# Optimization experiments

Measured on AMD Instinct MI355X. Metric: run time of the kernel, lower is better.

Reference implementation:

```python
import jax, jax.numpy as jnp
import numpy as np

B, S, D_MODEL, H = 4, 2048, 2048, 16
HD = D_MODEL // H  # 128
ROPE_BASE = 10000.0


def apply_rope(x):
    # x: [B, H, S, HD]; interleaved-pair rotary embedding along seq axis
    s, d = x.shape[2], x.shape[3]
    inv_freq = 1.0 / (ROPE_BASE ** (jnp.arange(0, d, 2, dtype=jnp.float32) / d))  # [d/2]
    ang = jnp.arange(s, dtype=jnp.float32)[:, None] * inv_freq[None, :]  # [S, d/2]
    cos, sin = jnp.cos(ang), jnp.sin(ang)
    x0, x1 = x[..., 0::2], x[..., 1::2]  # [B,H,S,d/2]
    o0 = x0 * cos - x1 * sin
    o1 = x0 * sin + x1 * cos
    return jnp.stack([o0, o1], axis=-1).reshape(x.shape)


def setup_inputs() -> dict:
    key = jax.random.key(0)
    ks = jax.random.split(key, 5)
    sc = 1.0 / np.sqrt(D_MODEL)
    return {
        "x": jax.random.normal(ks[0], (B, S, D_MODEL), dtype=jnp.float32),
        "Wq": jax.random.normal(ks[1], (D_MODEL, D_MODEL), dtype=jnp.float32) * sc,
        "Wk": jax.random.normal(ks[2], (D_MODEL, D_MODEL), dtype=jnp.float32) * sc,
        "Wv": jax.random.normal(ks[3], (D_MODEL, D_MODEL), dtype=jnp.float32) * sc,
        "Wo": jax.random.normal(ks[4], (D_MODEL, D_MODEL), dtype=jnp.float32) * sc,
        "bo": jnp.zeros((D_MODEL,), dtype=jnp.float32),
    }


def reference(x, Wq, Wk, Wv, Wo, bo):
    b, s, _ = x.shape
    # torch Linear: y = x @ W.T (no qkv bias)
    q = (x @ Wq.T).reshape(b, s, H, HD).transpose(0, 2, 1, 3)  # [B,H,S,HD]
    k = (x @ Wk.T).reshape(b, s, H, HD).transpose(0, 2, 1, 3)
    v = (x @ Wv.T).reshape(b, s, H, HD).transpose(0, 2, 1, 3)
    q = apply_rope(q)
    k = apply_rope(k)
    scores = jnp.einsum("bhqd,bhkd->bhqk", q, k)
    causal = jnp.tril(jnp.ones((s, s), dtype=bool))
    scores = jnp.where(causal, scores, -jnp.inf)
    attn = jax.nn.softmax(scores / jnp.sqrt(jnp.float32(HD)), axis=-1)
    # dropout p=0.0 -> identity
    ctx = jnp.einsum("bhqk,bhkd->bqhd", attn, v).reshape(b, s, H * HD)
    return ctx @ Wo.T + bo
```

## Files before the change

kernel.cpp:

```cpp
#include <hip/hip_runtime.h>
#include <hip/hip_bf16.h>
#include <math.h>

#define B_  4
#define S_  2048
#define DM  2048
#define H_  16
#define HD_ 128

typedef __bf16 bf16;
typedef __bf16 bf16x4 __attribute__((ext_vector_type(4)));
typedef __bf16 bf16x8 __attribute__((ext_vector_type(8)));
typedef float  f32x4  __attribute__((ext_vector_type(4)));

__device__ __forceinline__ void gload_lds16(const bf16* g, bf16* l) {
  __builtin_amdgcn_global_load_lds(
      (const __attribute__((address_space(1))) void*)g,
      (__attribute__((address_space(3))) void*)l, 16, 0, 0);
}

#define NX4 4194304
#define NW4 1048576
__global__ void cast_all(const float* __restrict__ x, const float* __restrict__ wq,
                         const float* __restrict__ wk, const float* __restrict__ wv,
                         const float* __restrict__ wo,
                         bf16* __restrict__ xb, bf16* __restrict__ wqkv,
                         bf16* __restrict__ wob) {
  const int total = NX4 + 4 * NW4;
  int stride = gridDim.x * blockDim.x;
  for (int i = blockIdx.x * blockDim.x + threadIdx.x; i < total; i += stride) {
    const float* src; bf16* dst; int j;
    if (i < NX4) { src = x; dst = xb; j = i; }
    else {
      int t = i - NX4; int r = t >> 20; j = t & (NW4 - 1);
      if      (r == 0) { src = wq; dst = wqkv; }
      else if (r == 1) { src = wk; dst = wqkv + (size_t)NW4 * 4; }
      else if (r == 2) { src = wv; dst = wqkv + (size_t)NW4 * 8; }
      else             { src = wo; dst = wob; }
    }
    float4 v = reinterpret_cast<const float4*>(src)[j];
    bf16x4 o = { (bf16)v.x, (bf16)v.y, (bf16)v.z, (bf16)v.w };
    reinterpret_cast<bf16x4*>(dst)[j] = o;
  }
}

__global__ void rope_table_k(float* __restrict__ tab) {
  int idx = blockIdx.x * blockDim.x + threadIdx.x;
  if (idx >= S_ * (HD_ / 2)) return;
  int pos = idx >> 6, i = idx & 63;
  float inv = powf(10000.0f, -(2.0f * i) / (float)HD_);
  float ang = (float)pos * inv;
  tab[2 * idx]     = cosf(ang);
  tab[2 * idx + 1] = sinf(ang);
}

template<int EPI>
__global__ __launch_bounds__(512, 2)
void gemm16d(const bf16* __restrict__ A, const bf16* __restrict__ Bt,
             bf16* __restrict__ Oq, bf16* __restrict__ Ok, bf16* __restrict__ Ovt,
             float* __restrict__ Cf, const float* __restrict__ bias,
             const float* __restrict__ tab, int N, int K) {
  __shared__ char lds[131072];
  const int tid = threadIdx.x;
  const int w = tid >> 6, l = tid & 63;
  const int lr = l & 15, lg = l >> 4;
  const int wm = w >> 2, wn = w & 3;
  const int row0 = blockIdx.y * 256, col0 = blockIdx.x * 256;
  const int NT = K >> 6;

  auto stageSlot = [&](int isB, int kh, int kt2) {
    const bf16* src = isB ? (Bt + (size_t)col0 * K) : (A + (size_t)row0 * K);
    char* dstbase = (char*)lds + (kt2 & 1) * 65536 + isB * 32768 + kh * 16384;
    const int kcol = kt2 * 64 + kh * 32;
#pragma unroll
    for (int u = 0; u < 2; ++u) {
      int D = w * 2048 + u * 1024 + l * 16;
      int r = D >> 6, cb = D & 63;
      int sc = cb ^ (((r >> 1) & 3) << 4);
      gload_lds16(src + (size_t)r * K + kcol + (sc >> 1),
                  (bf16*)(dstbase + w * 2048 + u * 1024));
    }
  };

  const int swzt = ((lr >> 1) & 3) << 4;
  int offA[2][4], offB[4];
#pragma unroll
  for (int qm = 0; qm < 2; ++qm)
#pragma unroll
    for (int mi = 0; mi < 4; ++mi) {
      int r = wm * 128 + qm * 64 + mi * 16 + lr;
      offA[qm][mi] = r * 64 + ((lg * 16) ^ swzt);
    }
#pragma unroll
  for (int ni = 0; ni < 4; ++ni) {
    int r = wn * 64 + ni * 16 + lr;
    offB[ni] = 32768 + r * 64 + ((lg * 16) ^ swzt);
  }

  f32x4 acc[8][4] = {};

  stageSlot(0, 0, 0); stageSlot(1, 0, 0);
  stageSlot(0, 1, 0); stageSlot(1, 1, 0);
  if (NT > 1) { stageSlot(0, 0, 1); stageSlot(1, 0, 1); }
  asm volatile("s_waitcnt vmcnt(8)" ::: "memory");
  __builtin_amdgcn_s_barrier();

#pragma unroll 1
  for (int kt = 0; kt < NT; ++kt) {
    const char* bufb = (const char*)lds + (kt & 1) * 65536;
#pragma unroll
    for (int kh = 0; kh < 2; ++kh) {
      const char* bb = bufb + kh * 16384;
      bf16x8 af[4], bfr[4];
#pragma unroll
      for (int ni = 0; ni < 4; ++ni)
        bfr[ni] = *reinterpret_cast<const bf16x8*>(bb + offB[ni]);
#pragma unroll
      for (int mi = 0; mi < 4; ++mi)
        af[mi] = *reinterpret_cast<const bf16x8*>(bb + offA[0][mi]);
      if (kh == 0) { if (kt + 1 < NT) stageSlot(0, 1, kt + 1); }
      else         { if (kt + 2 < NT) stageSlot(0, 0, kt + 2); }
      __builtin_amdgcn_s_barrier();
      __builtin_amdgcn_s_setprio(1);
#pragma unroll
      for (int mi = 0; mi < 4; ++mi)
#pragma unroll
        for (int ni = 0; ni < 4; ++ni)
          acc[mi][ni] = __builtin_amdgcn_mfma_f32_16x16x32_bf16(af[mi], bfr[ni], acc[mi][ni], 0, 0, 0);
      __builtin_amdgcn_s_setprio(0);
#pragma unroll
      for (int mi = 0; mi < 4; ++mi)
        af[mi] = *reinterpret_cast<const bf16x8*>(bb + offA[1][mi]);
      if (kh == 0) {
        if (kt + 1 < NT) stageSlot(1, 1, kt + 1);
        if (kt == NT - 1) asm volatile("s_waitcnt vmcnt(0)" ::: "memory");
        else              asm volatile("s_waitcnt vmcnt(8)" ::: "memory");
      } else {
        if (kt + 2 < NT) stageSlot(1, 0, kt + 2);
        if (kt < NT - 1) {
          if (kt == NT - 2) asm volatile("s_waitcnt vmcnt(4)" ::: "memory");
          else              asm volatile("s_waitcnt vmcnt(8)" ::: "memory");
        }
      }
      __builtin_amdgcn_s_barrier();
      __builtin_amdgcn_s_setprio(1);
#pragma unroll
      for (int mi = 0; mi < 4; ++mi)
#pragma unroll
        for (int ni = 0; ni < 4; ++ni)
          acc[4 + mi][ni] = __builtin_amdgcn_mfma_f32_16x16x32_bf16(af[mi], bfr[ni], acc[4 + mi][ni], 0, 0, 0);
      __builtin_amdgcn_s_setprio(0);
    }
  }

#pragma unroll
  for (int ai = 0; ai < 8; ++ai) {
    int rb = row0 + wm * 128 + ai * 16 + lg * 4;
#pragma unroll
    for (int ni = 0; ni < 4; ++ni) {
      int gc = col0 + wn * 64 + ni * 16 + lr;
      if (EPI == 1) {
#pragma unroll
        for (int j = 0; j < 4; ++j)
          Cf[(size_t)(rb + j) * N + gc] = acc[ai][ni][j] + bias[gc];
      } else {
        int reg = col0 >> 11;
        int cc = gc & 2047;
        if (reg == 2) {
          int bb2 = rb >> 11, ss = rb & 2047;
          int hh = cc >> 7, dd = cc & 127;
          bf16x4 pack = { (bf16)acc[ai][ni][0], (bf16)acc[ai][ni][1],
                          (bf16)acc[ai][ni][2], (bf16)acc[ai][ni][3] };
          *reinterpret_cast<bf16x4*>(Ovt + (((size_t)(bb2 * H_ + hh) * HD_ + dd) << 11) + ss) = pack;
        } else {
          bf16* Dst = (reg == 0) ? Oq : Ok;
          float scale = (reg == 0) ? 0.08838834764831845f : 1.0f;
          int i2 = (cc & 127) >> 1;
          float sgn = (lr & 1) ? 1.0f : -1.0f;
#pragma unroll
          for (int j = 0; j < 4; ++j) {
            float own = acc[ai][ni][j];
            float par = __shfl_xor(own, 1);
            int ss = (rb + j) & (S_ - 1);
            float2 cs = reinterpret_cast<const float2*>(tab)[ss * 64 + i2];
            Dst[(size_t)(rb + j) * 2048 + cc] = (bf16)((own * cs.x + sgn * par * cs.y) * scale);
          }
        }
      }
    }
  }
}

__global__ __launch_bounds__(512, 4)
void attn_fwd(const bf16* __restrict__ Q, const bf16* __restrict__ K,
              const bf16* __restrict__ Vt, bf16* __restrict__ O) {
  __shared__ bf16 Ks[2][64 * 128];
  __shared__ bf16 Vs[2][128 * 64];
  __shared__ bf16 Ps[8][16 * 64];
  const int tid = threadIdx.x;
  const int w = tid >> 6, l = tid & 63;
  const int lr = l & 15, lg = l >> 4;
  const int L = blockIdx.x + 8 * (blockIdx.y + 16 * blockIdx.z);
  const int xcd = L & 7, s = L >> 3;
  const int p = xcd * 8 + (s & 7);
  const int bx = s >> 3;
  const int h = p & 15, b = p >> 4;
  const size_t bbase = (size_t)b * S_ * DM + (size_t)h * HD_;
  const bf16* vtb = Vt + (size_t)(b * H_ + h) * HD_ * S_;

#pragma unroll 1
  for (int pass = 0; pass < 2; ++pass) {
    const int qt = pass ? bx : (15 - bx);
    const int q0 = qt * 128 + w * 16;
    const int ktmax = 2 * qt + 1;

    bf16x8 qf[4];
#pragma unroll
    for (int kb = 0; kb < 4; ++kb)
      qf[kb] = *reinterpret_cast<const bf16x8*>(Q + bbase + (size_t)(q0 + lr) * DM + kb * 32 + lg * 8);

    float m_r = -INFINITY;
    float l_r = 0.f;
    f32x4 o[8] = {};

#pragma unroll
    for (int i = 0; i < 2; ++i) {
      int X = w * 2048 + i * 1024 + l * 16;
      int r = X >> 8, scb = (X & 255) ^ ((r & 7) << 4);
      gload_lds16(K + bbase + (size_t)r * DM + (scb >> 1), &Ks[0][(w * 2048 + i * 1024) >> 1]);
    }
#pragma unroll
    for (int i = 0; i < 2; ++i) {
      int X = w * 2048 + i * 1024 + l * 16;
      int d = X >> 7, scb = (X & 127) ^ ((d & 7) << 4);
      gload_lds16(vtb + (size_t)d * S_ + (scb >> 1), &Vs[0][(w * 2048 + i * 1024) >> 1]);
    }

    for (int kt = 0; kt <= ktmax; ++kt) {
      const int buf = kt & 1;
      if (kt < ktmax) {
        const int nk = (kt + 1) * 64;
#pragma unroll
        for (int i = 0; i < 2; ++i) {
          int X = w * 2048 + i * 1024 + l * 16;
          int r = X >> 8, scb = (X & 255) ^ ((r & 7) << 4);
          gload_lds16(K + bbase + (size_t)(nk + r) * DM + (scb >> 1),
                      &Ks[buf ^ 1][(w * 2048 + i * 1024) >> 1]);
        }
#pragma unroll
        for (int i = 0; i < 2; ++i) {
          int X = w * 2048 + i * 1024 + l * 16;
          int d = X >> 7, scb = (X & 127) ^ ((d & 7) << 4);
          gload_lds16(vtb + (size_t)d * S_ + nk + (scb >> 1),
                      &Vs[buf ^ 1][(w * 2048 + i * 1024) >> 1]);
        }
        asm volatile("s_waitcnt vmcnt(4)" ::: "memory");
      } else {
        asm volatile("s_waitcnt vmcnt(0)" ::: "memory");
      }
      __builtin_amdgcn_s_barrier();

      f32x4 sc4[4];
      __builtin_amdgcn_s_setprio(1);
#pragma unroll
      for (int cb = 0; cb < 4; ++cb) {
        sc4[cb] = f32x4{0.f, 0.f, 0.f, 0.f};
        int r = cb * 16 + lr;
#pragma unroll
        for (int kb = 0; kb < 4; ++kb) {
          int off = r * 256 + ((kb * 64 + lg * 16) ^ ((lr & 7) << 4));
          bf16x8 kf = *reinterpret_cast<const bf16x8*>((const char*)Ks[buf] + off);
          sc4[cb] = __builtin_amdgcn_mfma_f32_16x16x32_bf16(kf, qf[kb], sc4[cb], 0, 0, 0);
        }
      }
      __builtin_amdgcn_s_setprio(0);

      const int kv0 = kt * 64;
      if (kv0 + 63 > q0) {
        const int qq = q0 + lr;
#pragma unroll
        for (int cb = 0; cb < 4; ++cb)
#pragma unroll
          for (int jj = 0; jj < 4; ++jj)
            if (kv0 + cb * 16 + lg * 4 + jj > qq) sc4[cb][jj] = -INFINITY;
      }

      float tm = -INFINITY;
#pragma unroll
      for (int cb = 0; cb < 4; ++cb)
#pragma unroll
        for (int jj = 0; jj < 4; ++jj) tm = fmaxf(tm, sc4[cb][jj]);
      tm = fmaxf(tm, __shfl_xor(tm, 16));
      tm = fmaxf(tm, __shfl_xor(tm, 32));
      const bool resc = !__all(tm <= m_r + 8.0f);
      float sc_f = 1.f;
      if (resc) {
        float mnew = fmaxf(m_r, tm);
        sc_f = __expf(m_r - mnew);
        m_r = mnew;
      }
      float rs = 0.f;
#pragma unroll
      for (int cb = 0; cb < 4; ++cb)
#pragma unroll
        for (int jj = 0; jj < 4; ++jj) {
          float pp = __expf(sc4[cb][jj] - m_r);
          sc4[cb][jj] = pp;
          rs += pp;
        }
      rs += __shfl_xor(rs, 16);
      rs += __shfl_xor(rs, 32);
      l_r = l_r * sc_f + rs;
      if (resc) {
        float scO[4];
#pragma unroll
        for (int j = 0; j < 4; ++j) scO[j] = __shfl(sc_f, lg * 4 + j);
#pragma unroll
        for (int nb = 0; nb < 8; ++nb)
#pragma unroll
          for (int j = 0; j < 4; ++j) o[nb][j] *= scO[j];
      }

#pragma unroll
      for (int cb = 0; cb < 4; ++cb) {
        bf16x4 pk = { (bf16)sc4[cb][0], (bf16)sc4[cb][1], (bf16)sc4[cb][2], (bf16)sc4[cb][3] };
        int off = lr * 128 + ((cb * 32 + lg * 8) ^ ((lr & 7) << 4));
        *reinterpret_cast<bf16x4*>((char*)Ps[w] + off) = pk;
      }

      bf16x8 pf[2];
#pragma unroll
      for (int kc = 0; kc < 2; ++kc) {
        int off = lr * 128 + ((kc * 64 + lg * 16) ^ ((lr & 7) << 4));
        pf[kc] = *reinterpret_cast<const bf16x8*>((const char*)Ps[w] + off);
      }
      __builtin_amdgcn_s_setprio(1);
#pragma unroll
      for (int nb = 0; nb < 8; ++nb) {
        int d = nb * 16 + lr;
#pragma unroll
        for (int kc = 0; kc < 2; ++kc) {
          int off = d * 128 + ((kc * 64 + lg * 16) ^ ((lr & 7) << 4));
          bf16x8 vf = *reinterpret_cast<const bf16x8*>((const char*)Vs[buf] + off);
          o[nb] = __builtin_amdgcn_mfma_f32_16x16x32_bf16(pf[kc], vf, o[nb], 0, 0, 0);
        }
      }
      __builtin_amdgcn_s_setprio(0);

      asm volatile("s_waitcnt lgkmcnt(0)" ::: "memory");
      __builtin_amdgcn_s_barrier();
    }

    float lO[4];
#pragma unroll
    for (int j = 0; j < 4; ++j) lO[j] = __shfl(l_r, lg * 4 + j);
#pragma unroll
    for (int j = 0; j < 4; ++j) {
      float inv = 1.0f / lO[j];
      size_t rowoff = bbase + (size_t)(q0 + lg * 4 + j) * DM;
#pragma unroll
      for (int nb = 0; nb < 8; ++nb)
        O[rowoff + nb * 16 + lr] = (bf16)(o[nb][j] * inv);
    }
  }
}

extern "C" void kernel_launch(void* const* d_in, const int* in_sizes, int n_in,
                              void* d_out, int out_size, void* d_ws, size_t ws_size,
                              hipStream_t stream) {
  const float* x  = (const float*)d_in[0];
  const float* Wq = (const float*)d_in[1];
  const float* Wk = (const float*)d_in[2];
  const float* Wv = (const float*)d_in[3];
  const float* Wo = (const float*)d_in[4];
  const float* bo = (const float*)d_in[5];
  float* out = (float*)d_out;

  const size_t NX = (size_t)B_ * S_ * DM;
  const size_t NW = (size_t)DM * DM;
  char* ws = (char*)d_ws;
  bf16* xb   = (bf16*)ws; ws += NX * 2;
  bf16* wqkv = (bf16*)ws; ws += 3 * NW * 2;
  bf16* wob  = (bf16*)ws; ws += NW * 2;
  bf16* qb   = (bf16*)ws; ws += NX * 2;
  bf16* kb   = (bf16*)ws; ws += NX * 2;
  bf16* vt   = (bf16*)ws; ws += NX * 2;
  bf16* ctxb = (bf16*)ws; ws += NX * 2;
  float* tab = (float*)ws; ws += (size_t)S_ * 64 * 2 * sizeof(float);

  cast_all<<<2048, 256, 0, stream>>>(x, Wq, Wk, Wv, Wo, xb, wqkv, wob);
  rope_table_k<<<(S_ * 64 + 255) / 256, 256, 0, stream>>>(tab);

  const int M = B_ * S_;
  gemm16d<0><<<dim3(3 * DM / 256, M / 256), 512, 0, stream>>>(
      xb, wqkv, qb, kb, vt, nullptr, nullptr, tab, 3 * DM, DM);

  attn_fwd<<<dim3(8, H_, B_), 512, 0, stream>>>(qb, kb, vt, ctxb);

  gemm16d<1><<<dim3(DM / 256, M / 256), 512, 0, stream>>>(
      ctxb, wob, nullptr, nullptr, nullptr, out, bo, nullptr, DM, DM);
}
```

Measured before the change: 402.7 us.

## Double attention query tile per wave to reuse K/V fragments across two row blocks

Each wave now processes 32 query rows (two 16-row MFMA blocks) instead of 16, so each K and V fragment read from LDS feeds two MFMAs. The block query tile grows from 128 to 256 rows and the grid halves. The per-block K/V loads are therefore amortised over twice the queries, cutting LDS and global traffic per FLOP. In exchange, register pressure roughly doubles (launch bounds lowered to 2 blocks per CU), only 256 blocks are launched, and causal load balance across fewer, larger tiles gets coarser.

```diff
diff --git a/kernel.cpp b/kernel.cpp
--- a/kernel.cpp
+++ b/kernel.cpp
@@ -191,16 +191,16 @@
   }
 }
 
-__global__ __launch_bounds__(512, 4)
+__global__ __launch_bounds__(512, 2)
 void attn_fwd(const bf16* __restrict__ Q, const bf16* __restrict__ K,
               const bf16* __restrict__ Vt, bf16* __restrict__ O) {
   __shared__ bf16 Ks[2][64 * 128];
   __shared__ bf16 Vs[2][128 * 64];
-  __shared__ bf16 Ps[8][16 * 64];
+  __shared__ bf16 Ps[8][32 * 64];
   const int tid = threadIdx.x;
   const int w = tid >> 6, l = tid & 63;
   const int lr = l & 15, lg = l >> 4;
-  const int L = blockIdx.x + 8 * (blockIdx.y + 16 * blockIdx.z);
+  const int L = blockIdx.x + 4 * (blockIdx.y + 16 * blockIdx.z);
   const int xcd = L & 7, s = L >> 3;
   const int p = xcd * 8 + (s & 7);
   const int bx = s >> 3;
@@ -210,18 +210,21 @@
 
 #pragma unroll 1
   for (int pass = 0; pass < 2; ++pass) {
-    const int qt = pass ? bx : (15 - bx);
-    const int q0 = qt * 128 + w * 16;
-    const int ktmax = 2 * qt + 1;
-
-    bf16x8 qf[4];
-#pragma unroll
-    for (int kb = 0; kb < 4; ++kb)
-      qf[kb] = *reinterpret_cast<const bf16x8*>(Q + bbase + (size_t)(q0 + lr) * DM + kb * 32 + lg * 8);
-
-    float m_r = -INFINITY;
-    float l_r = 0.f;
-    f32x4 o[8] = {};
+    const int qt = pass ? bx : (7 - bx);
+    const int q0 = qt * 256 + w * 32;
+    const int ktmax = 4 * qt + 3;
+
+    bf16x8 qf[2][4];
+#pragma unroll
+    for (int qr = 0; qr < 2; ++qr)
+#pragma unroll
+      for (int kb = 0; kb < 4; ++kb)
+        qf[qr][kb] = *reinterpret_cast<const bf16x8*>(
+            Q + bbase + (size_t)(q0 + qr * 16 + lr) * DM + kb * 32 + lg * 8);
+
+    float m_r[2] = {-INFINITY, -INFINITY};
+    float l_r[2] = {0.f, 0.f};
+    f32x4 o[8][2] = {};
 
 #pragma unroll
     for (int i = 0; i < 2; ++i) {
@@ -260,80 +263,102 @@
       }
       __builtin_amdgcn_s_barrier();
 
-      f32x4 sc4[4];
+      f32x4 sc4[4][2];
       __builtin_amdgcn_s_setprio(1);
 #pragma unroll
       for (int cb = 0; cb < 4; ++cb) {
-        sc4[cb] = f32x4{0.f, 0.f, 0.f, 0.f};
+        sc4[cb][0] = f32x4{0.f, 0.f, 0.f, 0.f};
+        sc4[cb][1] = f32x4{0.f, 0.f, 0.f, 0.f};
         int r = cb * 16 + lr;
 #pragma unroll
         for (int kb = 0; kb < 4; ++kb) {
           int off = r * 256 + ((kb * 64 + lg * 16) ^ ((lr & 7) << 4));
           bf16x8 kf = *reinterpret_cast<const bf16x8*>((const char*)Ks[buf] + off);
-          sc4[cb] = __builtin_amdgcn_mfma_f32_16x16x32_bf16(kf, qf[kb], sc4[cb], 0, 0, 0);
+          sc4[cb][0] = __builtin_amdgcn_mfma_f32_16x16x32_bf16(kf, qf[0][kb], sc4[cb][0], 0, 0, 0);
+          sc4[cb][1] = __builtin_amdgcn_mfma_f32_16x16x32_bf16(kf, qf[1][kb], sc4[cb][1], 0, 0, 0);
         }
       }
       __builtin_amdgcn_s_setprio(0);
 
       const int kv0 = kt * 64;
       if (kv0 + 63 > q0) {
-        const int qq = q0 + lr;
+#pragma unroll
+        for (int qr = 0; qr < 2; ++qr) {
+          const int qq = q0 + qr * 16 + lr;
+#pragma unroll
+          for (int cb = 0; cb < 4; ++cb)
+#pragma unroll
+            for (int jj = 0; jj < 4; ++jj)
+              if (kv0 + cb * 16 + lg * 4 + jj > qq) sc4[cb][qr][jj] = -INFINITY;
+        }
+      }
+
+      float tm[2] = {-INFINITY, -INFINITY};
+#pragma unroll
+      for (int qr = 0; qr < 2; ++qr) {
 #pragma unroll
         for (int cb = 0; cb < 4; ++cb)
 #pragma unroll
-          for (int jj = 0; jj < 4; ++jj)
-            if (kv0 + cb * 16 + lg * 4 + jj > qq) sc4[cb][jj] = -INFINITY;
-      }
-
-      float tm = -INFINITY;
-#pragma unroll
-      for (int cb = 0; cb < 4; ++cb)
-#pragma unroll
-        for (int jj = 0; jj < 4; ++jj) tm = fmaxf(tm, sc4[cb][jj]);
-      tm = fmaxf(tm, __shfl_xor(tm, 16));
-      tm = fmaxf(tm, __shfl_xor(tm, 32));
-      const bool resc = !__all(tm <= m_r + 8.0f);
-      float sc_f = 1.f;
+          for (int jj = 0; jj < 4; ++jj) tm[qr] = fmaxf(tm[qr], sc4[cb][qr][jj]);
+        tm[qr] = fmaxf(tm[qr], __shfl_xor(tm[qr], 16));
+        tm[qr] = fmaxf(tm[qr], __shfl_xor(tm[qr], 32));
+      }
+      const bool resc = !__all(fmaxf(tm[0] - m_r[0], tm[1] - m_r[1]) <= 8.0f);
+      float sc_f[2] = {1.f, 1.f};
       if (resc) {
-        float mnew = fmaxf(m_r, tm);
-        sc_f = __expf(m_r - mnew);
-        m_r = mnew;
-      }
-      float rs = 0.f;
-#pragma unroll
-      for (int cb = 0; cb < 4; ++cb)
-#pragma unroll
-        for (int jj = 0; jj < 4; ++jj) {
-          float pp = __expf(sc4[cb][jj] - m_r);
-          sc4[cb][jj] = pp;
-          rs += pp;
-        }
-      rs += __shfl_xor(rs, 16);
-      rs += __shfl_xor(rs, 32);
-      l_r = l_r * sc_f + rs;
+#pragma unroll
+        for (int qr = 0; qr < 2; ++qr) {
+          float mnew = fmaxf(m_r[qr], tm[qr]);
+          sc_f[qr] = __expf(m_r[qr] - mnew);
+          m_r[qr] = mnew;
+        }
+      }
+#pragma unroll
+      for (int qr = 0; qr < 2; ++qr) {
+        float rs = 0.f;
+#pragma unroll
+        for (int cb = 0; cb < 4; ++cb)
+#pragma unroll
+          for (int jj = 0; jj < 4; ++jj) {
+            float pp = __expf(sc4[cb][qr][jj] - m_r[qr]);
+            sc4[cb][qr][jj] = pp;
+            rs += pp;
+          }
+        rs += __shfl_xor(rs, 16);
+        rs += __shfl_xor(rs, 32);
+        l_r[qr] = l_r[qr] * sc_f[qr] + rs;
+      }
       if (resc) {
-        float scO[4];
-#pragma unroll
-        for (int j = 0; j < 4; ++j) scO[j] = __shfl(sc_f, lg * 4 + j);
-#pragma unroll
-        for (int nb = 0; nb < 8; ++nb)
-#pragma unroll
-          for (int j = 0; j < 4; ++j) o[nb][j] *= scO[j];
-      }
-
-#pragma unroll
-      for (int cb = 0; cb < 4; ++cb) {
-        bf16x4 pk = { (bf16)sc4[cb][0], (bf16)sc4[cb][1], (bf16)sc4[cb][2], (bf16)sc4[cb][3] };
-        int off = lr * 128 + ((cb * 32 + lg * 8) ^ ((lr & 7) << 4));
-        *reinterpret_cast<bf16x4*>((char*)Ps[w] + off) = pk;
-      }
-
-      bf16x8 pf[2];
-#pragma unroll
-      for (int kc = 0; kc < 2; ++kc) {
-        int off = lr * 128 + ((kc * 64 + lg * 16) ^ ((lr & 7) << 4));
-        pf[kc] = *reinterpret_cast<const bf16x8*>((const char*)Ps[w] + off);
-      }
+#pragma unroll
+        for (int qr = 0; qr < 2; ++qr) {
+          float scO[4];
+#pragma unroll
+          for (int j = 0; j < 4; ++j) scO[j] = __shfl(sc_f[qr], lg * 4 + j);
+#pragma unroll
+          for (int nb = 0; nb < 8; ++nb)
+#pragma unroll
+            for (int j = 0; j < 4; ++j) o[nb][qr][j] *= scO[j];
+        }
+      }
+
+#pragma unroll
+      for (int qr = 0; qr < 2; ++qr)
+#pragma unroll
+        for (int cb = 0; cb < 4; ++cb) {
+          bf16x4 pk = { (bf16)sc4[cb][qr][0], (bf16)sc4[cb][qr][1],
+                        (bf16)sc4[cb][qr][2], (bf16)sc4[cb][qr][3] };
+          int off = (qr * 16 + lr) * 128 + ((cb * 32 + lg * 8) ^ ((lr & 7) << 4));
+          *reinterpret_cast<bf16x4*>((char*)Ps[w] + off) = pk;
+        }
+
+      bf16x8 pf[2][2];
+#pragma unroll
+      for (int qr = 0; qr < 2; ++qr)
+#pragma unroll
+        for (int kc = 0; kc < 2; ++kc) {
+          int off = (qr * 16 + lr) * 128 + ((kc * 64 + lg * 16) ^ ((lr & 7) << 4));
+          pf[qr][kc] = *reinterpret_cast<const bf16x8*>((const char*)Ps[w] + off);
+        }
       __builtin_amdgcn_s_setprio(1);
 #pragma unroll
       for (int nb = 0; nb < 8; ++nb) {
@@ -342,7 +367,8 @@
         for (int kc = 0; kc < 2; ++kc) {
           int off = d * 128 + ((kc * 64 + lg * 16) ^ ((lr & 7) << 4));
           bf16x8 vf = *reinterpret_cast<const bf16x8*>((const char*)Vs[buf] + off);
-          o[nb] = __builtin_amdgcn_mfma_f32_16x16x32_bf16(pf[kc], vf, o[nb], 0, 0, 0);
+          o[nb][0] = __builtin_amdgcn_mfma_f32_16x16x32_bf16(pf[0][kc], vf, o[nb][0], 0, 0, 0);
+          o[nb][1] = __builtin_amdgcn_mfma_f32_16x16x32_bf16(pf[1][kc], vf, o[nb][1], 0, 0, 0);
         }
       }
       __builtin_amdgcn_s_setprio(0);
@@ -351,16 +377,19 @@
       __builtin_amdgcn_s_barrier();
     }
 
-    float lO[4];
-#pragma unroll
-    for (int j = 0; j < 4; ++j) lO[j] = __shfl(l_r, lg * 4 + j);
-#pragma unroll
-    for (int j = 0; j < 4; ++j) {
-      float inv = 1.0f / lO[j];
-      size_t rowoff = bbase + (size_t)(q0 + lg * 4 + j) * DM;
-#pragma unroll
-      for (int nb = 0; nb < 8; ++nb)
-        O[rowoff + nb * 16 + lr] = (bf16)(o[nb][j] * inv);
+#pragma unroll
+    for (int qr = 0; qr < 2; ++qr) {
+      float lO[4];
+#pragma unroll
+      for (int j = 0; j < 4; ++j) lO[j] = __shfl(l_r[qr], lg * 4 + j);
+#pragma unroll
+      for (int j = 0; j < 4; ++j) {
+        float inv = 1.0f / lO[j];
+        size_t rowoff = bbase + (size_t)(q0 + qr * 16 + lg * 4 + j) * DM;
+#pragma unroll
+        for (int nb = 0; nb < 8; ++nb)
+          O[rowoff + nb * 16 + lr] = (bf16)(o[nb][qr][j] * inv);
+      }
     }
   }
 }
@@ -395,7 +424,7 @@
   gemm16d<0><<<dim3(3 * DM / 256, M / 256), 512, 0, stream>>>(
       xb, wqkv, qb, kb, vt, nullptr, nullptr, tab, 3 * DM, DM);
 
-  attn_fwd<<<dim3(8, H_, B_), 512, 0, stream>>>(qb, kb, vt, ctxb);
+  attn_fwd<<<dim3(4, H_, B_), 512, 0, stream>>>(qb, kb, vt, ctxb);
 
   gemm16d<1><<<dim3(DM / 256, M / 256), 512, 0, stream>>>(
       ctxb, wob, nullptr, nullptr, nullptr, out, bo, nullptr, DM, DM);
```

Result: no change. 406.3 us (+0.9%).
